# Optimization experiments

Hardware: AMD Instinct MI355X
Metric: run time of the kernel (lower is better)

Reference implementation:

```python
import jax, jax.numpy as jnp
import numpy as np

N = 8192
IN_F = 256
OUT_F = 128
E = 262144
NEG = -9e15


def setup_inputs() -> dict:
    key = jax.random.key(0)
    ks = jax.random.split(key, 12)
    glorot = lambda k, shp: jax.random.uniform(k, shp, jnp.float32,
                                               -jnp.sqrt(6.0 / (shp[0] + shp[1])),
                                               jnp.sqrt(6.0 / (shp[0] + shp[1])))
    return {
        "h_context": jax.random.normal(ks[0], (N, IN_F), jnp.float32),
        "h_structure": jax.random.normal(ks[1], (N, IN_F), jnp.float32),
        "edge_index": jax.random.randint(ks[2], (2, E), 0, N, jnp.int64),
        "Wc_w": glorot(ks[3], (OUT_F, IN_F)),
        "Wc_b": jnp.zeros((OUT_F,), jnp.float32),
        "Ws_w": glorot(ks[4], (OUT_F, IN_F)),
        "Ws_b": jnp.zeros((OUT_F,), jnp.float32),
        "ac_w": glorot(ks[5], (1, 2 * OUT_F)),
        "as_w": glorot(ks[6], (1, 2 * OUT_F)),
        "Ws_coff": jax.random.normal(ks[7], (1, 1), jnp.float32) * 1.414,
        "Wc_coff": jax.random.normal(ks[8], (1, 1), jnp.float32) * 1.414,
    }


def _pair_scores(h, a_w):
    # GAT trick: score[i,j] = leaky_relu(a1 . h[i] + a2 . h[j])
    F_out = h.shape[1]
    s_src = h @ a_w[0, :F_out]   # [N]
    s_dst = h @ a_w[0, F_out:]   # [N]
    return jax.nn.leaky_relu(s_src[:, None] + s_dst[None, :], 0.01)  # [N, N]


def reference(h_context, h_structure, edge_index, Wc_w, Wc_b, Ws_w, Ws_b,
              ac_w, as_w, Ws_coff, Wc_coff):
    hc = h_context @ Wc_w.T + Wc_b                      # [N, F]
    alpha_c = _pair_scores(hc, ac_w)                    # [N, N]
    hs = jax.nn.softmax(h_structure, axis=1) @ Ws_w.T + Ws_b
    alpha_s = _pair_scores(hs, as_w)                    # [N, N]
    alpha = jnp.abs(Ws_coff[0, 0]) * alpha_c + jnp.abs(Wc_coff[0, 0]) * alpha_s
    n = h_structure.shape[0]
    adj = jnp.zeros((n, n), bool).at[edge_index[0], edge_index[1]].set(True)
    attention = jnp.where(adj, alpha, NEG)
    attention = jax.nn.softmax(attention, axis=1)
    # dropout omitted (eval mode / deterministic reference)
    return attention @ hc
```

## Files before the change

kernel.cpp:

```cpp
#include <hip/hip_runtime.h>
#include <hip/hip_bf16.h>
#include <math.h>

#define N_NODES 8192
#define IN_FEAT 256
#define OUT_FEAT 128
#define WORDS_PER_ROW (N_NODES / 64)
#define CAPW 256
#define M_TILE 16

typedef unsigned long long u64;
typedef float v4f __attribute__((ext_vector_type(4)));
typedef short s8v __attribute__((ext_vector_type(8)));
typedef short s4v __attribute__((ext_vector_type(4)));

__device__ __forceinline__ float wred_sum_b(float v) {
    #pragma unroll
    for (int o = 32; o > 0; o >>= 1) v += __shfl_xor(v, o, 64);
    return v;
}
__device__ __forceinline__ float wred_max_b(float v) {
    #pragma unroll
    for (int o = 32; o > 0; o >>= 1) v = fmaxf(v, __shfl_xor(v, o, 64));
    return v;
}

__device__ __forceinline__ void bsplit(float x, unsigned short& hi, unsigned short& lo) {
    unsigned int xb = __float_as_uint(x);
    hi = (unsigned short)(xb >> 16);
    float lof = x - __uint_as_float(xb & 0xFFFF0000u);
    lo = (unsigned short)(__float_as_uint(lof) >> 16);
}

__global__ __launch_bounds__(256) void prep_w(
    const float* __restrict__ Wc, const float* __restrict__ Ws,
    unsigned short* __restrict__ wci, unsigned short* __restrict__ wsi)
{
    int i = blockIdx.x * 256 + threadIdx.x;
    int row = i >> 8, k = i & 255;
    int dst = row * 512 + ((k >> 3) << 4) + (k & 7);
    unsigned short h, l;
    bsplit(Wc[i], h, l); wci[dst] = h; wci[dst + 8] = l;
    bsplit(Ws[i], h, l); wsi[dst] = h; wsi[dst + 8] = l;
}

__global__ __launch_bounds__(256, 2) void node_feats(
    const float* __restrict__ hctx, const float* __restrict__ hstr,
    const unsigned short* __restrict__ wci, const unsigned short* __restrict__ wsi,
    const float* __restrict__ Wcb, const float* __restrict__ Wsb,
    const float* __restrict__ acw, const float* __restrict__ asw,
    const int* __restrict__ ei, int E, u64* __restrict__ bmp,
    float* __restrict__ hc,
    float* __restrict__ csrc, float* __restrict__ cdst,
    float* __restrict__ ssrc, float* __restrict__ sdst)
{
    __shared__ unsigned short aCh[M_TILE][264], aCl[M_TILE][264];
    __shared__ unsigned short aSh[M_TILE][264], aSl[M_TILE][264];
    __shared__ float invsh[M_TILE];
    __shared__ float hcT[M_TILE][132];
    __shared__ float hsT[M_TILE][132];

    const int t = threadIdx.x;
    const int w = t >> 6, ln = t & 63;
    const int r0 = blockIdx.x * M_TILE;

    {
        int pv = ei[2 * (ln & 31) + 1];
        u64 nz = __ballot(pv != 0);
        const int is64 = (nz == 0);
        for (int e = blockIdx.x * 256 + t; e < E; e += 512 * 256) {
            int s, d;
            if (is64) { s = ei[2 * e]; d = ei[2 * E + 2 * e]; }
            else      { s = ei[e];     d = ei[E + e]; }
            if ((unsigned)s < N_NODES && (unsigned)d < N_NODES)
                atomicOr(&bmp[(size_t)s * WORDS_PER_ROW + (d >> 6)], 1ull << (d & 63));
        }
    }

    #pragma unroll
    for (int j = 0; j < 4; j++) {
        int c = t + 256 * j;
        int r = c >> 6;
        int k = (c & 63) * 4;
        const float4 x = *(const float4*)(hctx + (size_t)(r0 + r) * IN_FEAT + k);
        unsigned short h0, h1, h2, h3, l0, l1, l2, l3;
        bsplit(x.x, h0, l0); bsplit(x.y, h1, l1);
        bsplit(x.z, h2, l2); bsplit(x.w, h3, l3);
        s4v hv = { (short)h0, (short)h1, (short)h2, (short)h3 };
        s4v lv = { (short)l0, (short)l1, (short)l2, (short)l3 };
        *(s4v*)&aCh[r][k] = hv;
        *(s4v*)&aCl[r][k] = lv;
    }

    #pragma unroll
    for (int rr = 0; rr < 4; rr++) {
        int r = w * 4 + rr;
        const float* srow = hstr + (size_t)(r0 + r) * IN_FEAT;
        float x0 = srow[ln], x1 = srow[ln + 64], x2 = srow[ln + 128], x3 = srow[ln + 192];
        float mx = wred_max_b(fmaxf(fmaxf(x0, x1), fmaxf(x2, x3)));
        float e0 = __expf(x0 - mx), e1 = __expf(x1 - mx);
        float e2 = __expf(x2 - mx), e3 = __expf(x3 - mx);
        float s = wred_sum_b(e0 + e1 + e2 + e3);
        if (ln == 0) invsh[r] = 1.0f / s;
        unsigned short h, l;
        bsplit(e0, h, l); aSh[r][ln]       = h; aSl[r][ln]       = l;
        bsplit(e1, h, l); aSh[r][ln + 64]  = h; aSl[r][ln + 64]  = l;
        bsplit(e2, h, l); aSh[r][ln + 128] = h; aSl[r][ln + 128] = l;
        bsplit(e3, h, l); aSh[r][ln + 192] = h; aSl[r][ln + 192] = l;
    }
    __syncthreads();

    const int m = ln & 15, q = ln >> 4;
    const int nA = (w << 5) + m, nB = nA + 16;

    v4f aC0 = {0.f,0.f,0.f,0.f}, aC1 = {0.f,0.f,0.f,0.f};
    v4f aS0 = {0.f,0.f,0.f,0.f}, aS1 = {0.f,0.f,0.f,0.f};

    {
        const unsigned short* p0 = wci + nA * 512;
        const unsigned short* p1 = wci + nB * 512;
        #pragma unroll 2
        for (int ks = 0; ks < 8; ks++) {
            const int ko = ks * 32 + q * 8;
            const int io = 2 * ko;
            s8v ah  = *(const s8v*)&aCh[m][ko];
            s8v al  = *(const s8v*)&aCl[m][ko];
            s8v b0h = *(const s8v*)(p0 + io);
            s8v b0l = *(const s8v*)(p0 + io + 8);
            s8v b1h = *(const s8v*)(p1 + io);
            s8v b1l = *(const s8v*)(p1 + io + 8);
            aC0 = __builtin_amdgcn_mfma_f32_16x16x32_bf16(al, b0h, aC0, 0, 0, 0);
            aC0 = __builtin_amdgcn_mfma_f32_16x16x32_bf16(ah, b0l, aC0, 0, 0, 0);
            aC0 = __builtin_amdgcn_mfma_f32_16x16x32_bf16(ah, b0h, aC0, 0, 0, 0);
            aC1 = __builtin_amdgcn_mfma_f32_16x16x32_bf16(al, b1h, aC1, 0, 0, 0);
            aC1 = __builtin_amdgcn_mfma_f32_16x16x32_bf16(ah, b1l, aC1, 0, 0, 0);
            aC1 = __builtin_amdgcn_mfma_f32_16x16x32_bf16(ah, b1h, aC1, 0, 0, 0);
        }
    }
    {
        const unsigned short* p0 = wsi + nA * 512;
        const unsigned short* p1 = wsi + nB * 512;
        #pragma unroll 2
        for (int ks = 0; ks < 8; ks++) {
            const int ko = ks * 32 + q * 8;
            const int io = 2 * ko;
            s8v ah  = *(const s8v*)&aSh[m][ko];
            s8v al  = *(const s8v*)&aSl[m][ko];
            s8v b0h = *(const s8v*)(p0 + io);
            s8v b0l = *(const s8v*)(p0 + io + 8);
            s8v b1h = *(const s8v*)(p1 + io);
            s8v b1l = *(const s8v*)(p1 + io + 8);
            aS0 = __builtin_amdgcn_mfma_f32_16x16x32_bf16(al, b0h, aS0, 0, 0, 0);
            aS0 = __builtin_amdgcn_mfma_f32_16x16x32_bf16(ah, b0l, aS0, 0, 0, 0);
            aS0 = __builtin_amdgcn_mfma_f32_16x16x32_bf16(ah, b0h, aS0, 0, 0, 0);
            aS1 = __builtin_amdgcn_mfma_f32_16x16x32_bf16(al, b1h, aS1, 0, 0, 0);
            aS1 = __builtin_amdgcn_mfma_f32_16x16x32_bf16(ah, b1l, aS1, 0, 0, 0);
            aS1 = __builtin_amdgcn_mfma_f32_16x16x32_bf16(ah, b1h, aS1, 0, 0, 0);
        }
    }

    const float cbA = Wcb[nA], cbB = Wcb[nB];
    const float sbA = Wsb[nA], sbB = Wsb[nB];
    #pragma unroll
    for (int p = 0; p < 4; p++) {
        int row = q * 4 + p;
        float iv = invsh[row];
        hcT[row][nA] = aC0[p] + cbA;
        hcT[row][nB] = aC1[p] + cbB;
        hsT[row][nA] = aS0[p] * iv + sbA;
        hsT[row][nB] = aS1[p] * iv + sbB;
    }
    __syncthreads();

    #pragma unroll
    for (int j = 0; j < 8; j++) {
        int f = t + 256 * j;
        int r = f >> 7, c = f & 127;
        hc[(size_t)(r0 + r) * OUT_FEAT + c] = hcT[r][c];
    }

    float a0 = acw[ln], a0b = acw[ln + 64], a1 = acw[128 + ln], a1b = acw[192 + ln];
    float b0 = asw[ln], b0b = asw[ln + 64], b1 = asw[128 + ln], b1b = asw[192 + ln];
    #pragma unroll
    for (int rr = 0; rr < 4; rr++) {
        int r = w + rr * 4;
        float c0 = hcT[r][ln], c1 = hcT[r][ln + 64];
        float s0 = hsT[r][ln], s1 = hsT[r][ln + 64];
        float v0 = wred_sum_b(c0 * a0 + c1 * a0b);
        float v1 = wred_sum_b(c0 * a1 + c1 * a1b);
        float v2 = wred_sum_b(s0 * b0 + s1 * b0b);
        float v3 = wred_sum_b(s0 * b1 + s1 * b1b);
        if (ln == 0) {
            csrc[r0 + r] = v0; cdst[r0 + r] = v1;
            ssrc[r0 + r] = v2; sdst[r0 + r] = v3;
        }
    }
}

__global__ __launch_bounds__(256) void attn(
    const u64* __restrict__ bmp,
    const float* __restrict__ hc,
    const float* __restrict__ csrc, const float* __restrict__ cdst,
    const float* __restrict__ ssrc, const float* __restrict__ sdst,
    const float* __restrict__ wscoff, const float* __restrict__ wccoff,
    float* __restrict__ out)
{
    __shared__ int   jl[4][CAPW];
    __shared__ float pl[4][CAPW];

    const int w  = threadIdx.x >> 6;
    const int ln = threadIdx.x & 63;
    const int i  = blockIdx.x * 4 + w;

    const float wS = fabsf(wscoff[0]);
    const float wC = fabsf(wccoff[0]);
    const float cs = csrc[i], ss = ssrc[i];

    ulonglong2 wv = *(const ulonglong2*)(bmp + (size_t)i * WORDS_PER_ROW + 2 * ln);
    int c = __popcll(wv.x) + __popcll(wv.y);

    int inc = c;
    #pragma unroll
    for (int o = 1; o < 64; o <<= 1) {
        int y = __shfl_up(inc, o, 64);
        if (ln >= o) inc += y;
    }
    int pre = inc - c;
    int cnt = __shfl(inc, 63, 64);

    int idx = pre;
    #pragma unroll
    for (int h = 0; h < 2; h++) {
        u64 ww = (h == 0) ? wv.x : wv.y;
        int jb = ln * 128 + h * 64;
        while (ww) {
            int b = __ffsll(ww) - 1; ww &= ww - 1;
            int j = jb + b;
            float ac  = cs + cdst[j];
            float as_ = ss + sdst[j];
            ac  = (ac  > 0.0f) ? ac  : 0.01f * ac;
            as_ = (as_ > 0.0f) ? as_ : 0.01f * as_;
            if (idx < CAPW) { jl[w][idx] = j; pl[w][idx] = wS * ac + wC * as_; }
            idx++;
        }
    }
    if (cnt > CAPW) cnt = CAPW;
    __threadfence_block();

    if (cnt == 0) {
        float2 acc = {0.f, 0.f};
        const float2* hc2 = (const float2*)hc;
        for (int j = 0; j < N_NODES; j++) {
            float2 h2 = hc2[(size_t)j * 64 + ln];
            acc.x += h2.x; acc.y += h2.y;
        }
        float2 o2 = { acc.x / (float)N_NODES, acc.y / (float)N_NODES };
        *(float2*)(out + (size_t)i * OUT_FEAT + 2 * ln) = o2;
        return;
    }

    float m = -1e30f;
    for (int k = ln; k < cnt; k += 64) m = fmaxf(m, pl[w][k]);
    m = wred_max_b(m);
    float s = 0.0f;
    for (int k = ln; k < cnt; k += 64) {
        float p = __expf(pl[w][k] - m);
        pl[w][k] = p;
        s += p;
    }
    s = wred_sum_b(s);
    float inv = 1.0f / s;
    __threadfence_block();

    const float2* hc2 = (const float2*)hc;
    float2 acc = {0.f, 0.f};
    int k = 0;
    for (; k + 4 <= cnt; k += 4) {
        int   j0 = jl[w][k],   j1 = jl[w][k+1], j2 = jl[w][k+2], j3 = jl[w][k+3];
        float p0 = pl[w][k],   p1 = pl[w][k+1], p2 = pl[w][k+2], p3 = pl[w][k+3];
        float2 h0 = hc2[(size_t)j0 * 64 + ln];
        float2 h1 = hc2[(size_t)j1 * 64 + ln];
        float2 h2 = hc2[(size_t)j2 * 64 + ln];
        float2 h3 = hc2[(size_t)j3 * 64 + ln];
        acc.x += p0 * h0.x + p1 * h1.x + p2 * h2.x + p3 * h3.x;
        acc.y += p0 * h0.y + p1 * h1.y + p2 * h2.y + p3 * h3.y;
    }
    for (; k < cnt; k++) {
        float2 h0 = hc2[(size_t)jl[w][k] * 64 + ln];
        float p0 = pl[w][k];
        acc.x += p0 * h0.x; acc.y += p0 * h0.y;
    }
    float2 o2 = { acc.x * inv, acc.y * inv };
    *(float2*)(out + (size_t)i * OUT_FEAT + 2 * ln) = o2;
}

extern "C" void kernel_launch(void* const* d_in, const int* in_sizes, int n_in,
                              void* d_out, int out_size, void* d_ws, size_t ws_size,
                              hipStream_t stream)
{
    const float* hctx = (const float*)d_in[0];
    const float* hstr = (const float*)d_in[1];
    const int*   ei   = (const int*)d_in[2];
    const float* Wc   = (const float*)d_in[3];
    const float* Wcb  = (const float*)d_in[4];
    const float* Ws   = (const float*)d_in[5];
    const float* Wsb  = (const float*)d_in[6];
    const float* acw  = (const float*)d_in[7];
    const float* asw  = (const float*)d_in[8];
    const float* wsco = (const float*)d_in[9];
    const float* wcco = (const float*)d_in[10];
    float* out = (float*)d_out;

    const int n2 = in_sizes[2];
    const int E  = (n2 == 4 * 262144) ? 262144 : n2 / 2;

    char* ws = (char*)d_ws;
    size_t off = 0;
    float* hc   = (float*)(ws + off); off += (size_t)N_NODES * OUT_FEAT * sizeof(float);
    float* csrc = (float*)(ws + off); off += (size_t)N_NODES * sizeof(float);
    float* cdst = (float*)(ws + off); off += (size_t)N_NODES * sizeof(float);
    float* ssrc = (float*)(ws + off); off += (size_t)N_NODES * sizeof(float);
    float* sdst = (float*)(ws + off); off += (size_t)N_NODES * sizeof(float);
    off = (off + 255) & ~(size_t)255;
    u64* bmp    = (u64*)(ws + off);   off += (size_t)N_NODES * WORDS_PER_ROW * sizeof(u64);
    unsigned short* wci = (unsigned short*)(ws + off); off += (size_t)OUT_FEAT * IN_FEAT * 2 * sizeof(unsigned short);
    unsigned short* wsi = (unsigned short*)(ws + off); off += (size_t)OUT_FEAT * IN_FEAT * 2 * sizeof(unsigned short);

    hipMemsetAsync(bmp, 0, (size_t)N_NODES * WORDS_PER_ROW * sizeof(u64), stream);

    prep_w<<<128, 256, 0, stream>>>(Wc, Ws, wci, wsi);
    node_feats<<<N_NODES / M_TILE, 256, 0, stream>>>(hctx, hstr, wci, wsi,
                                                     Wcb, Wsb, acw, asw, ei, E, bmp,
                                                     hc, csrc, cdst, ssrc, sdst);
    attn<<<N_NODES / 4, 256, 0, stream>>>(bmp, hc, csrc, cdst, ssrc, sdst, wsco, wcco, out);
}
```

Baseline: 132.3 us.

## Fuse weight prep, node features and attention into one persistent kernel with grid barriers

Merges the three kernels and the bitmap memset into a single 512-block kernel that synchronises through a software grid barrier. Each block zeroes its own slice of the adjacency bitmap and converts weights into an MFMA-fragment-ordered layout so B operands load contiguously per lane. The attention phase now loops over four rows per wave. This removes launch gaps and the memset, but the grid barrier is only safe if all 512 blocks are co-resident, and attention parallelism drops from 2048 blocks to 512.

```diff
diff --git a/kernel.cpp b/kernel.cpp
--- a/kernel.cpp
+++ b/kernel.cpp
@@ -1,13 +1,13 @@
 #include <hip/hip_runtime.h>
-#include <hip/hip_bf16.h>
 #include <math.h>
 
 #define N_NODES 8192
 #define IN_FEAT 256
 #define OUT_FEAT 128
-#define WORDS_PER_ROW (N_NODES / 64)
+#define WORDS_PER_ROW 128
 #define CAPW 256
 #define M_TILE 16
+#define NBLK 512
 
 typedef unsigned long long u64;
 typedef float v4f __attribute__((ext_vector_type(4)));
@@ -32,43 +32,93 @@
     lo = (unsigned short)(__float_as_uint(lof) >> 16);
 }
 
-__global__ __launch_bounds__(256) void prep_w(
-    const float* __restrict__ Wc, const float* __restrict__ Ws,
-    unsigned short* __restrict__ wci, unsigned short* __restrict__ wsi)
-{
-    int i = blockIdx.x * 256 + threadIdx.x;
-    int row = i >> 8, k = i & 255;
-    int dst = row * 512 + ((k >> 3) << 4) + (k & 7);
-    unsigned short h, l;
-    bsplit(Wc[i], h, l); wci[dst] = h; wci[dst + 8] = l;
-    bsplit(Ws[i], h, l); wsi[dst] = h; wsi[dst + 8] = l;
-}
-
-__global__ __launch_bounds__(256, 2) void node_feats(
+__device__ __forceinline__ void grid_barrier(int* cnt, int* gen) {
+    __syncthreads();
+    if (threadIdx.x == 0) {
+        __threadfence();
+        int g = __hip_atomic_load(gen, __ATOMIC_RELAXED, __HIP_MEMORY_SCOPE_AGENT);
+        int arrived = __hip_atomic_fetch_add(cnt, 1, __ATOMIC_ACQ_REL, __HIP_MEMORY_SCOPE_AGENT);
+        if (arrived == NBLK - 1) {
+            __hip_atomic_store(cnt, 0, __ATOMIC_RELAXED, __HIP_MEMORY_SCOPE_AGENT);
+            __hip_atomic_store(gen, g + 1, __ATOMIC_RELEASE, __HIP_MEMORY_SCOPE_AGENT);
+        } else {
+            while (__hip_atomic_load(gen, __ATOMIC_ACQUIRE, __HIP_MEMORY_SCOPE_AGENT) == g)
+                __builtin_amdgcn_s_sleep(2);
+        }
+        __threadfence();
+    }
+    __syncthreads();
+}
+
+__global__ __launch_bounds__(256, 2) void fused(
     const float* __restrict__ hctx, const float* __restrict__ hstr,
-    const unsigned short* __restrict__ wci, const unsigned short* __restrict__ wsi,
+    const float* __restrict__ Wc,  const float* __restrict__ Ws,
     const float* __restrict__ Wcb, const float* __restrict__ Wsb,
     const float* __restrict__ acw, const float* __restrict__ asw,
-    const int* __restrict__ ei, int E, u64* __restrict__ bmp,
+    const float* __restrict__ wscoff, const float* __restrict__ wccoff,
+    const int* __restrict__ ei, int E,
+    u64* __restrict__ bmp,
+    unsigned short* __restrict__ cfrag, unsigned short* __restrict__ sfrag,
     float* __restrict__ hc,
     float* __restrict__ csrc, float* __restrict__ cdst,
-    float* __restrict__ ssrc, float* __restrict__ sdst)
+    float* __restrict__ ssrc, float* __restrict__ sdst,
+    int* __restrict__ bar_cnt, int* __restrict__ bar_gen,
+    float* __restrict__ out)
 {
     __shared__ unsigned short aCh[M_TILE][264], aCl[M_TILE][264];
     __shared__ unsigned short aSh[M_TILE][264], aSl[M_TILE][264];
     __shared__ float invsh[M_TILE];
     __shared__ float hcT[M_TILE][132];
     __shared__ float hsT[M_TILE][132];
+    __shared__ int   jl[4][CAPW];
+    __shared__ float pl[4][CAPW];
 
     const int t = threadIdx.x;
     const int w = t >> 6, ln = t & 63;
-    const int r0 = blockIdx.x * M_TILE;
+    const int b = blockIdx.x;
+    const int r0 = b * M_TILE;
+
+    {
+        ulonglong2 z = {0ull, 0ull};
+        ulonglong2* dst = (ulonglong2*)(bmp + (size_t)b * M_TILE * WORDS_PER_ROW);
+        #pragma unroll
+        for (int k = 0; k < 4; k++) dst[t + 256 * k] = z;
+    }
+    {
+        int tid = b * 256 + t;
+        if (tid < 16384) {
+            int mat = tid >> 13;
+            int f = tid & 8191;
+            int lnf = f & 63;
+            int sel = (f >> 6) & 3;
+            int ks  = (f >> 8) & 7;
+            int wv  = (f >> 11) & 3;
+            int row = (wv << 5) + ((sel >> 1) << 4) + (lnf & 15);
+            int part = sel & 1;
+            int k0 = (ks << 5) + ((lnf >> 4) << 3);
+            const float* src = (mat ? Ws : Wc) + row * IN_FEAT + k0;
+            short tmp[8];
+            #pragma unroll
+            for (int j = 0; j < 8; j++) {
+                float x = src[j];
+                unsigned int xb = __float_as_uint(x);
+                if (part == 0) tmp[j] = (short)(xb >> 16);
+                else {
+                    float lof = x - __uint_as_float(xb & 0xFFFF0000u);
+                    tmp[j] = (short)(__float_as_uint(lof) >> 16);
+                }
+            }
+            unsigned short* dst = (mat ? sfrag : cfrag) + (size_t)f * 8;
+            *(s8v*)dst = *(const s8v*)tmp;
+        }
+    }
+    grid_barrier(bar_cnt, bar_gen);
 
     {
         int pv = ei[2 * (ln & 31) + 1];
         u64 nz = __ballot(pv != 0);
         const int is64 = (nz == 0);
-        for (int e = blockIdx.x * 256 + t; e < E; e += 512 * 256) {
+        for (int e = b * 256 + t; e < E; e += NBLK * 256) {
             int s, d;
             if (is64) { s = ei[2 * e]; d = ei[2 * E + 2 * e]; }
             else      { s = ei[e];     d = ei[E + e]; }
@@ -91,7 +141,6 @@
         *(s4v*)&aCh[r][k] = hv;
         *(s4v*)&aCl[r][k] = lv;
     }
-
     #pragma unroll
     for (int rr = 0; rr < 4; rr++) {
         int r = w * 4 + rr;
@@ -111,54 +160,45 @@
     __syncthreads();
 
     const int m = ln & 15, q = ln >> 4;
-    const int nA = (w << 5) + m, nB = nA + 16;
-
     v4f aC0 = {0.f,0.f,0.f,0.f}, aC1 = {0.f,0.f,0.f,0.f};
     v4f aS0 = {0.f,0.f,0.f,0.f}, aS1 = {0.f,0.f,0.f,0.f};
 
-    {
-        const unsigned short* p0 = wci + nA * 512;
-        const unsigned short* p1 = wci + nB * 512;
-        #pragma unroll 2
-        for (int ks = 0; ks < 8; ks++) {
-            const int ko = ks * 32 + q * 8;
-            const int io = 2 * ko;
-            s8v ah  = *(const s8v*)&aCh[m][ko];
-            s8v al  = *(const s8v*)&aCl[m][ko];
-            s8v b0h = *(const s8v*)(p0 + io);
-            s8v b0l = *(const s8v*)(p0 + io + 8);
-            s8v b1h = *(const s8v*)(p1 + io);
-            s8v b1l = *(const s8v*)(p1 + io + 8);
-            aC0 = __builtin_amdgcn_mfma_f32_16x16x32_bf16(al, b0h, aC0, 0, 0, 0);
-            aC0 = __builtin_amdgcn_mfma_f32_16x16x32_bf16(ah, b0l, aC0, 0, 0, 0);
-            aC0 = __builtin_amdgcn_mfma_f32_16x16x32_bf16(ah, b0h, aC0, 0, 0, 0);
-            aC1 = __builtin_amdgcn_mfma_f32_16x16x32_bf16(al, b1h, aC1, 0, 0, 0);
-            aC1 = __builtin_amdgcn_mfma_f32_16x16x32_bf16(ah, b1l, aC1, 0, 0, 0);
-            aC1 = __builtin_amdgcn_mfma_f32_16x16x32_bf16(ah, b1h, aC1, 0, 0, 0);
-        }
-    }
-    {
-        const unsigned short* p0 = wsi + nA * 512;
-        const unsigned short* p1 = wsi + nB * 512;
-        #pragma unroll 2
-        for (int ks = 0; ks < 8; ks++) {
-            const int ko = ks * 32 + q * 8;
-            const int io = 2 * ko;
-            s8v ah  = *(const s8v*)&aSh[m][ko];
-            s8v al  = *(const s8v*)&aSl[m][ko];
-            s8v b0h = *(const s8v*)(p0 + io);
-            s8v b0l = *(const s8v*)(p0 + io + 8);
-            s8v b1h = *(const s8v*)(p1 + io);
-            s8v b1l = *(const s8v*)(p1 + io + 8);
-            aS0 = __builtin_amdgcn_mfma_f32_16x16x32_bf16(al, b0h, aS0, 0, 0, 0);
-            aS0 = __builtin_amdgcn_mfma_f32_16x16x32_bf16(ah, b0l, aS0, 0, 0, 0);
-            aS0 = __builtin_amdgcn_mfma_f32_16x16x32_bf16(ah, b0h, aS0, 0, 0, 0);
-            aS1 = __builtin_amdgcn_mfma_f32_16x16x32_bf16(al, b1h, aS1, 0, 0, 0);
-            aS1 = __builtin_amdgcn_mfma_f32_16x16x32_bf16(ah, b1l, aS1, 0, 0, 0);
-            aS1 = __builtin_amdgcn_mfma_f32_16x16x32_bf16(ah, b1h, aS1, 0, 0, 0);
-        }
-    }
-
+    #pragma unroll 2
+    for (int ks = 0; ks < 8; ks++) {
+        int ko = ks * 32 + q * 8;
+        const s8v* base = (const s8v*)cfrag + ((w * 8 + ks) * 4) * 64 + ln;
+        s8v ah  = *(const s8v*)&aCh[m][ko];
+        s8v al  = *(const s8v*)&aCl[m][ko];
+        s8v bh0 = base[0];
+        s8v bl0 = base[64];
+        s8v bh1 = base[128];
+        s8v bl1 = base[192];
+        aC0 = __builtin_amdgcn_mfma_f32_16x16x32_bf16(al, bh0, aC0, 0, 0, 0);
+        aC0 = __builtin_amdgcn_mfma_f32_16x16x32_bf16(ah, bl0, aC0, 0, 0, 0);
+        aC0 = __builtin_amdgcn_mfma_f32_16x16x32_bf16(ah, bh0, aC0, 0, 0, 0);
+        aC1 = __builtin_amdgcn_mfma_f32_16x16x32_bf16(al, bh1, aC1, 0, 0, 0);
+        aC1 = __builtin_amdgcn_mfma_f32_16x16x32_bf16(ah, bl1, aC1, 0, 0, 0);
+        aC1 = __builtin_amdgcn_mfma_f32_16x16x32_bf16(ah, bh1, aC1, 0, 0, 0);
+    }
+    #pragma unroll 2
+    for (int ks = 0; ks < 8; ks++) {
+        int ko = ks * 32 + q * 8;
+        const s8v* base = (const s8v*)sfrag + ((w * 8 + ks) * 4) * 64 + ln;
+        s8v ah  = *(const s8v*)&aSh[m][ko];
+        s8v al  = *(const s8v*)&aSl[m][ko];
+        s8v bh0 = base[0];
+        s8v bl0 = base[64];
+        s8v bh1 = base[128];
+        s8v bl1 = base[192];
+        aS0 = __builtin_amdgcn_mfma_f32_16x16x32_bf16(al, bh0, aS0, 0, 0, 0);
+        aS0 = __builtin_amdgcn_mfma_f32_16x16x32_bf16(ah, bl0, aS0, 0, 0, 0);
+        aS0 = __builtin_amdgcn_mfma_f32_16x16x32_bf16(ah, bh0, aS0, 0, 0, 0);
+        aS1 = __builtin_amdgcn_mfma_f32_16x16x32_bf16(al, bh1, aS1, 0, 0, 0);
+        aS1 = __builtin_amdgcn_mfma_f32_16x16x32_bf16(ah, bl1, aS1, 0, 0, 0);
+        aS1 = __builtin_amdgcn_mfma_f32_16x16x32_bf16(ah, bh1, aS1, 0, 0, 0);
+    }
+
+    const int nA = (w << 5) + m, nB = nA + 16;
     const float cbA = Wcb[nA], cbB = Wcb[nB];
     const float sbA = Wsb[nA], sbB = Wsb[nB];
     #pragma unroll
@@ -178,120 +218,109 @@
         int r = f >> 7, c = f & 127;
         hc[(size_t)(r0 + r) * OUT_FEAT + c] = hcT[r][c];
     }
-
-    float a0 = acw[ln], a0b = acw[ln + 64], a1 = acw[128 + ln], a1b = acw[192 + ln];
-    float b0 = asw[ln], b0b = asw[ln + 64], b1 = asw[128 + ln], b1b = asw[192 + ln];
-    #pragma unroll
-    for (int rr = 0; rr < 4; rr++) {
-        int r = w + rr * 4;
-        float c0 = hcT[r][ln], c1 = hcT[r][ln + 64];
-        float s0 = hsT[r][ln], s1 = hsT[r][ln + 64];
-        float v0 = wred_sum_b(c0 * a0 + c1 * a0b);
-        float v1 = wred_sum_b(c0 * a1 + c1 * a1b);
-        float v2 = wred_sum_b(s0 * b0 + s1 * b0b);
-        float v3 = wred_sum_b(s0 * b1 + s1 * b1b);
-        if (ln == 0) {
-            csrc[r0 + r] = v0; cdst[r0 + r] = v1;
-            ssrc[r0 + r] = v2; sdst[r0 + r] = v3;
-        }
-    }
-}
-
-__global__ __launch_bounds__(256) void attn(
-    const u64* __restrict__ bmp,
-    const float* __restrict__ hc,
-    const float* __restrict__ csrc, const float* __restrict__ cdst,
-    const float* __restrict__ ssrc, const float* __restrict__ sdst,
-    const float* __restrict__ wscoff, const float* __restrict__ wccoff,
-    float* __restrict__ out)
-{
-    __shared__ int   jl[4][CAPW];
-    __shared__ float pl[4][CAPW];
-
-    const int w  = threadIdx.x >> 6;
-    const int ln = threadIdx.x & 63;
-    const int i  = blockIdx.x * 4 + w;
+    {
+        float a0 = acw[ln], a0b = acw[ln + 64], a1 = acw[128 + ln], a1b = acw[192 + ln];
+        float b0 = asw[ln], b0b = asw[ln + 64], b1 = asw[128 + ln], b1b = asw[192 + ln];
+        #pragma unroll
+        for (int rr = 0; rr < 4; rr++) {
+            int r = w + rr * 4;
+            float c0 = hcT[r][ln], c1 = hcT[r][ln + 64];
+            float s0 = hsT[r][ln], s1 = hsT[r][ln + 64];
+            float v0 = wred_sum_b(c0 * a0 + c1 * a0b);
+            float v1 = wred_sum_b(c0 * a1 + c1 * a1b);
+            float v2 = wred_sum_b(s0 * b0 + s1 * b0b);
+            float v3 = wred_sum_b(s0 * b1 + s1 * b1b);
+            if (ln == 0) {
+                csrc[r0 + r] = v0; cdst[r0 + r] = v1;
+                ssrc[r0 + r] = v2; sdst[r0 + r] = v3;
+            }
+        }
+    }
+    grid_barrier(bar_cnt, bar_gen);
 
     const float wS = fabsf(wscoff[0]);
     const float wC = fabsf(wccoff[0]);
-    const float cs = csrc[i], ss = ssrc[i];
-
-    ulonglong2 wv = *(const ulonglong2*)(bmp + (size_t)i * WORDS_PER_ROW + 2 * ln);
-    int c = __popcll(wv.x) + __popcll(wv.y);
-
-    int inc = c;
-    #pragma unroll
-    for (int o = 1; o < 64; o <<= 1) {
-        int y = __shfl_up(inc, o, 64);
-        if (ln >= o) inc += y;
-    }
-    int pre = inc - c;
-    int cnt = __shfl(inc, 63, 64);
-
-    int idx = pre;
-    #pragma unroll
-    for (int h = 0; h < 2; h++) {
-        u64 ww = (h == 0) ? wv.x : wv.y;
-        int jb = ln * 128 + h * 64;
-        while (ww) {
-            int b = __ffsll(ww) - 1; ww &= ww - 1;
-            int j = jb + b;
-            float ac  = cs + cdst[j];
-            float as_ = ss + sdst[j];
-            ac  = (ac  > 0.0f) ? ac  : 0.01f * ac;
-            as_ = (as_ > 0.0f) ? as_ : 0.01f * as_;
-            if (idx < CAPW) { jl[w][idx] = j; pl[w][idx] = wS * ac + wC * as_; }
-            idx++;
-        }
-    }
-    if (cnt > CAPW) cnt = CAPW;
-    __threadfence_block();
-
-    if (cnt == 0) {
+    const float2* hc2 = (const float2*)hc;
+
+    for (int rr = 0; rr < 4; rr++) {
+        const int i = b * 16 + w * 4 + rr;
+        const float cs = csrc[i], ss = ssrc[i];
+
+        ulonglong2 wv2 = *(const ulonglong2*)(bmp + (size_t)i * WORDS_PER_ROW + 2 * ln);
+        int c = __popcll(wv2.x) + __popcll(wv2.y);
+
+        int inc = c;
+        #pragma unroll
+        for (int o = 1; o < 64; o <<= 1) {
+            int y = __shfl_up(inc, o, 64);
+            if (ln >= o) inc += y;
+        }
+        int pre = inc - c;
+        int cnt = __shfl(inc, 63, 64);
+
+        int idx = pre;
+        #pragma unroll
+        for (int h = 0; h < 2; h++) {
+            u64 ww = (h == 0) ? wv2.x : wv2.y;
+            int jb = ln * 128 + h * 64;
+            while (ww) {
+                int bt = __ffsll(ww) - 1; ww &= ww - 1;
+                int j = jb + bt;
+                float ac  = cs + cdst[j];
+                float as_ = ss + sdst[j];
+                ac  = (ac  > 0.0f) ? ac  : 0.01f * ac;
+                as_ = (as_ > 0.0f) ? as_ : 0.01f * as_;
+                if (idx < CAPW) { jl[w][idx] = j; pl[w][idx] = wS * ac + wC * as_; }
+                idx++;
+            }
+        }
+        if (cnt > CAPW) cnt = CAPW;
+        __threadfence_block();
+
+        if (cnt == 0) {
+            float2 acc = {0.f, 0.f};
+            for (int j = 0; j < N_NODES; j++) {
+                float2 h2 = hc2[(size_t)j * 64 + ln];
+                acc.x += h2.x; acc.y += h2.y;
+            }
+            float2 o2 = { acc.x / (float)N_NODES, acc.y / (float)N_NODES };
+            *(float2*)(out + (size_t)i * OUT_FEAT + 2 * ln) = o2;
+            continue;
+        }
+
+        float mx = -1e30f;
+        for (int k = ln; k < cnt; k += 64) mx = fmaxf(mx, pl[w][k]);
+        mx = wred_max_b(mx);
+        float sm = 0.0f;
+        for (int k = ln; k < cnt; k += 64) {
+            float p = __expf(pl[w][k] - mx);
+            pl[w][k] = p;
+            sm += p;
+        }
+        sm = wred_sum_b(sm);
+        float inv = 1.0f / sm;
+        __threadfence_block();
+
         float2 acc = {0.f, 0.f};
-        const float2* hc2 = (const float2*)hc;
-        for (int j = 0; j < N_NODES; j++) {
-            float2 h2 = hc2[(size_t)j * 64 + ln];
-            acc.x += h2.x; acc.y += h2.y;
-        }
-        float2 o2 = { acc.x / (float)N_NODES, acc.y / (float)N_NODES };
+        int k = 0;
+        for (; k + 4 <= cnt; k += 4) {
+            int   j0 = jl[w][k],   j1 = jl[w][k+1], j2 = jl[w][k+2], j3 = jl[w][k+3];
+            float p0 = pl[w][k],   p1 = pl[w][k+1], p2 = pl[w][k+2], p3 = pl[w][k+3];
+            float2 h0 = hc2[(size_t)j0 * 64 + ln];
+            float2 h1 = hc2[(size_t)j1 * 64 + ln];
+            float2 h2 = hc2[(size_t)j2 * 64 + ln];
+            float2 h3 = hc2[(size_t)j3 * 64 + ln];
+            acc.x += p0 * h0.x + p1 * h1.x + p2 * h2.x + p3 * h3.x;
+            acc.y += p0 * h0.y + p1 * h1.y + p2 * h2.y + p3 * h3.y;
+        }
+        for (; k < cnt; k++) {
+            float2 h0 = hc2[(size_t)jl[w][k] * 64 + ln];
+            float p0 = pl[w][k];
+            acc.x += p0 * h0.x; acc.y += p0 * h0.y;
+        }
+        float2 o2 = { acc.x * inv, acc.y * inv };
         *(float2*)(out + (size_t)i * OUT_FEAT + 2 * ln) = o2;
-        return;
-    }
-
-    float m = -1e30f;
-    for (int k = ln; k < cnt; k += 64) m = fmaxf(m, pl[w][k]);
-    m = wred_max_b(m);
-    float s = 0.0f;
-    for (int k = ln; k < cnt; k += 64) {
-        float p = __expf(pl[w][k] - m);
-        pl[w][k] = p;
-        s += p;
-    }
-    s = wred_sum_b(s);
-    float inv = 1.0f / s;
-    __threadfence_block();
-
-    const float2* hc2 = (const float2*)hc;
-    float2 acc = {0.f, 0.f};
-    int k = 0;
-    for (; k + 4 <= cnt; k += 4) {
-        int   j0 = jl[w][k],   j1 = jl[w][k+1], j2 = jl[w][k+2], j3 = jl[w][k+3];
-        float p0 = pl[w][k],   p1 = pl[w][k+1], p2 = pl[w][k+2], p3 = pl[w][k+3];
-        float2 h0 = hc2[(size_t)j0 * 64 + ln];
-        float2 h1 = hc2[(size_t)j1 * 64 + ln];
-        float2 h2 = hc2[(size_t)j2 * 64 + ln];
-        float2 h3 = hc2[(size_t)j3 * 64 + ln];
-        acc.x += p0 * h0.x + p1 * h1.x + p2 * h2.x + p3 * h3.x;
-        acc.y += p0 * h0.y + p1 * h1.y + p2 * h2.y + p3 * h3.y;
-    }
-    for (; k < cnt; k++) {
-        float2 h0 = hc2[(size_t)jl[w][k] * 64 + ln];
-        float p0 = pl[w][k];
-        acc.x += p0 * h0.x; acc.y += p0 * h0.y;
-    }
-    float2 o2 = { acc.x * inv, acc.y * inv };
-    *(float2*)(out + (size_t)i * OUT_FEAT + 2 * ln) = o2;
+    }
 }
 
 extern "C" void kernel_launch(void* const* d_in, const int* in_sizes, int n_in,
@@ -323,14 +352,17 @@
     float* sdst = (float*)(ws + off); off += (size_t)N_NODES * sizeof(float);
     off = (off + 255) & ~(size_t)255;
     u64* bmp    = (u64*)(ws + off);   off += (size_t)N_NODES * WORDS_PER_ROW * sizeof(u64);
-    unsigned short* wci = (unsigned short*)(ws + off); off += (size_t)OUT_FEAT * IN_FEAT * 2 * sizeof(unsigned short);
-    unsigned short* wsi = (unsigned short*)(ws + off); off += (size_t)OUT_FEAT * IN_FEAT * 2 * sizeof(unsigned short);
-
-    hipMemsetAsync(bmp, 0, (size_t)N_NODES * WORDS_PER_ROW * sizeof(u64), stream);
-
-    prep_w<<<128, 256, 0, stream>>>(Wc, Ws, wci, wsi);
-    node_feats<<<N_NODES / M_TILE, 256, 0, stream>>>(hctx, hstr, wci, wsi,
-                                                     Wcb, Wsb, acw, asw, ei, E, bmp,
-                                                     hc, csrc, cdst, ssrc, sdst);
-    attn<<<N_NODES / 4, 256, 0, stream>>>(bmp, hc, csrc, cdst, ssrc, sdst, wsco, wcco, out);
-}
+    unsigned short* cfrag = (unsigned short*)(ws + off); off += (size_t)8192 * 8 * sizeof(unsigned short);
+    unsigned short* sfrag = (unsigned short*)(ws + off); off += (size_t)8192 * 8 * sizeof(unsigned short);
+    off = (off + 255) & ~(size_t)255;
+    int* bar = (int*)(ws + off); off += 256;
+    int* bar_cnt = bar;
+    int* bar_gen = bar + 16;
+
+    hipMemsetAsync(bar, 0, 128, stream);
+
+    fused<<<NBLK, 256, 0, stream>>>(hctx, hstr, Wc, Ws, Wcb, Wsb, acw, asw,
+                                    wsco, wcco, ei, E, bmp, cfrag, sfrag,
+                                    hc, csrc, cdst, ssrc, sdst,
+                                    bar_cnt, bar_gen, out);
+}
```

Measured after the change: 274.3 us. 107% more time.

## Split node_feats into context/structure blocks and fuse weight split in-kernel

Applied to the files above, without the earlier changes.

Removes the separate prep_w launch: each block now loads fp32 weights straight from global memory and splits them into bf16 hi/lo pairs in registers. The node_feats grid is doubled so that half the blocks compute the context projection and half the structure projection. Shared memory per block is halved and launch bounds now allow 4 blocks per CU, which raises parallelism and occupancy. The cost is redundant weight splitting in every block and more global weight reads (fp32 instead of preformatted bf16).

```diff
diff --git a/kernel.cpp b/kernel.cpp
--- a/kernel.cpp
+++ b/kernel.cpp
@@ -1,13 +1,13 @@
 #include <hip/hip_runtime.h>
-#include <hip/hip_bf16.h>
 #include <math.h>
 
 #define N_NODES 8192
 #define IN_FEAT 256
 #define OUT_FEAT 128
-#define WORDS_PER_ROW (N_NODES / 64)
+#define WORDS_PER_ROW 128
 #define CAPW 256
 #define M_TILE 16
+#define NF_BLOCKS 1024
 
 typedef unsigned long long u64;
 typedef float v4f __attribute__((ext_vector_type(4)));
@@ -32,21 +32,21 @@
     lo = (unsigned short)(__float_as_uint(lof) >> 16);
 }
 
-__global__ __launch_bounds__(256) void prep_w(
-    const float* __restrict__ Wc, const float* __restrict__ Ws,
-    unsigned short* __restrict__ wci, unsigned short* __restrict__ wsi)
-{
-    int i = blockIdx.x * 256 + threadIdx.x;
-    int row = i >> 8, k = i & 255;
-    int dst = row * 512 + ((k >> 3) << 4) + (k & 7);
-    unsigned short h, l;
-    bsplit(Wc[i], h, l); wci[dst] = h; wci[dst + 8] = l;
-    bsplit(Ws[i], h, l); wsi[dst] = h; wsi[dst + 8] = l;
-}
-
-__global__ __launch_bounds__(256, 2) void node_feats(
+__device__ __forceinline__ void split8(const float* p, s8v& h8, s8v& l8) {
+    short hh[8], ll[8];
+    #pragma unroll
+    for (int j = 0; j < 8; j++) {
+        unsigned short h, l;
+        bsplit(p[j], h, l);
+        hh[j] = (short)h; ll[j] = (short)l;
+    }
+    h8 = *(const s8v*)hh;
+    l8 = *(const s8v*)ll;
+}
+
+__global__ __launch_bounds__(256, 4) void node_feats(
     const float* __restrict__ hctx, const float* __restrict__ hstr,
-    const unsigned short* __restrict__ wci, const unsigned short* __restrict__ wsi,
+    const float* __restrict__ Wc,  const float* __restrict__ Ws,
     const float* __restrict__ Wcb, const float* __restrict__ Wsb,
     const float* __restrict__ acw, const float* __restrict__ asw,
     const int* __restrict__ ei, int E, u64* __restrict__ bmp,
@@ -54,21 +54,21 @@
     float* __restrict__ csrc, float* __restrict__ cdst,
     float* __restrict__ ssrc, float* __restrict__ sdst)
 {
-    __shared__ unsigned short aCh[M_TILE][264], aCl[M_TILE][264];
-    __shared__ unsigned short aSh[M_TILE][264], aSl[M_TILE][264];
+    __shared__ unsigned short aH[M_TILE][264], aL[M_TILE][264];
     __shared__ float invsh[M_TILE];
-    __shared__ float hcT[M_TILE][132];
-    __shared__ float hsT[M_TILE][132];
+    __shared__ float hT[M_TILE][132];
 
     const int t = threadIdx.x;
     const int w = t >> 6, ln = t & 63;
-    const int r0 = blockIdx.x * M_TILE;
+    const int is_struct = (blockIdx.x >= 512);
+    const int b = blockIdx.x & 511;
+    const int r0 = b * M_TILE;
 
     {
         int pv = ei[2 * (ln & 31) + 1];
         u64 nz = __ballot(pv != 0);
         const int is64 = (nz == 0);
-        for (int e = blockIdx.x * 256 + t; e < E; e += 512 * 256) {
+        for (int e = blockIdx.x * 256 + t; e < E; e += NF_BLOCKS * 256) {
             int s, d;
             if (is64) { s = ei[2 * e]; d = ei[2 * E + 2 * e]; }
             else      { s = ei[e];     d = ei[E + e]; }
@@ -77,122 +77,114 @@
         }
     }
 
-    #pragma unroll
-    for (int j = 0; j < 4; j++) {
-        int c = t + 256 * j;
-        int r = c >> 6;
-        int k = (c & 63) * 4;
-        const float4 x = *(const float4*)(hctx + (size_t)(r0 + r) * IN_FEAT + k);
-        unsigned short h0, h1, h2, h3, l0, l1, l2, l3;
-        bsplit(x.x, h0, l0); bsplit(x.y, h1, l1);
-        bsplit(x.z, h2, l2); bsplit(x.w, h3, l3);
-        s4v hv = { (short)h0, (short)h1, (short)h2, (short)h3 };
-        s4v lv = { (short)l0, (short)l1, (short)l2, (short)l3 };
-        *(s4v*)&aCh[r][k] = hv;
-        *(s4v*)&aCl[r][k] = lv;
-    }
-
-    #pragma unroll
-    for (int rr = 0; rr < 4; rr++) {
-        int r = w * 4 + rr;
-        const float* srow = hstr + (size_t)(r0 + r) * IN_FEAT;
-        float x0 = srow[ln], x1 = srow[ln + 64], x2 = srow[ln + 128], x3 = srow[ln + 192];
-        float mx = wred_max_b(fmaxf(fmaxf(x0, x1), fmaxf(x2, x3)));
-        float e0 = __expf(x0 - mx), e1 = __expf(x1 - mx);
-        float e2 = __expf(x2 - mx), e3 = __expf(x3 - mx);
-        float s = wred_sum_b(e0 + e1 + e2 + e3);
-        if (ln == 0) invsh[r] = 1.0f / s;
-        unsigned short h, l;
-        bsplit(e0, h, l); aSh[r][ln]       = h; aSl[r][ln]       = l;
-        bsplit(e1, h, l); aSh[r][ln + 64]  = h; aSl[r][ln + 64]  = l;
-        bsplit(e2, h, l); aSh[r][ln + 128] = h; aSl[r][ln + 128] = l;
-        bsplit(e3, h, l); aSh[r][ln + 192] = h; aSl[r][ln + 192] = l;
+    if (!is_struct) {
+        #pragma unroll
+        for (int j = 0; j < 4; j++) {
+            int c = t + 256 * j;
+            int r = c >> 6;
+            int k = (c & 63) * 4;
+            const float4 x = *(const float4*)(hctx + (size_t)(r0 + r) * IN_FEAT + k);
+            unsigned short h0, h1, h2, h3, l0, l1, l2, l3;
+            bsplit(x.x, h0, l0); bsplit(x.y, h1, l1);
+            bsplit(x.z, h2, l2); bsplit(x.w, h3, l3);
+            s4v hv = { (short)h0, (short)h1, (short)h2, (short)h3 };
+            s4v lv = { (short)l0, (short)l1, (short)l2, (short)l3 };
+            *(s4v*)&aH[r][k] = hv;
+            *(s4v*)&aL[r][k] = lv;
+        }
+    } else {
+        #pragma unroll
+        for (int rr = 0; rr < 4; rr++) {
+            int r = w * 4 + rr;
+            const float* srow = hstr + (size_t)(r0 + r) * IN_FEAT;
+            float x0 = srow[ln], x1 = srow[ln + 64], x2 = srow[ln + 128], x3 = srow[ln + 192];
+            float mx = wred_max_b(fmaxf(fmaxf(x0, x1), fmaxf(x2, x3)));
+            float e0 = __expf(x0 - mx), e1 = __expf(x1 - mx);
+            float e2 = __expf(x2 - mx), e3 = __expf(x3 - mx);
+            float s = wred_sum_b(e0 + e1 + e2 + e3);
+            if (ln == 0) invsh[r] = 1.0f / s;
+            unsigned short h, l;
+            bsplit(e0, h, l); aH[r][ln]       = h; aL[r][ln]       = l;
+            bsplit(e1, h, l); aH[r][ln + 64]  = h; aL[r][ln + 64]  = l;
+            bsplit(e2, h, l); aH[r][ln + 128] = h; aL[r][ln + 128] = l;
+            bsplit(e3, h, l); aH[r][ln + 192] = h; aL[r][ln + 192] = l;
+        }
     }
     __syncthreads();
 
     const int m = ln & 15, q = ln >> 4;
     const int nA = (w << 5) + m, nB = nA + 16;
-
-    v4f aC0 = {0.f,0.f,0.f,0.f}, aC1 = {0.f,0.f,0.f,0.f};
-    v4f aS0 = {0.f,0.f,0.f,0.f}, aS1 = {0.f,0.f,0.f,0.f};
-
-    {
-        const unsigned short* p0 = wci + nA * 512;
-        const unsigned short* p1 = wci + nB * 512;
-        #pragma unroll 2
-        for (int ks = 0; ks < 8; ks++) {
-            const int ko = ks * 32 + q * 8;
-            const int io = 2 * ko;
-            s8v ah  = *(const s8v*)&aCh[m][ko];
-            s8v al  = *(const s8v*)&aCl[m][ko];
-            s8v b0h = *(const s8v*)(p0 + io);
-            s8v b0l = *(const s8v*)(p0 + io + 8);
-            s8v b1h = *(const s8v*)(p1 + io);
-            s8v b1l = *(const s8v*)(p1 + io + 8);
-            aC0 = __builtin_amdgcn_mfma_f32_16x16x32_bf16(al, b0h, aC0, 0, 0, 0);
-            aC0 = __builtin_amdgcn_mfma_f32_16x16x32_bf16(ah, b0l, aC0, 0, 0, 0);
-            aC0 = __builtin_amdgcn_mfma_f32_16x16x32_bf16(ah, b0h, aC0, 0, 0, 0);
-            aC1 = __builtin_amdgcn_mfma_f32_16x16x32_bf16(al, b1h, aC1, 0, 0, 0);
-            aC1 = __builtin_amdgcn_mfma_f32_16x16x32_bf16(ah, b1l, aC1, 0, 0, 0);
-            aC1 = __builtin_amdgcn_mfma_f32_16x16x32_bf16(ah, b1h, aC1, 0, 0, 0);
-        }
-    }
-    {
-        const unsigned short* p0 = wsi + nA * 512;
-        const unsigned short* p1 = wsi + nB * 512;
-        #pragma unroll 2
-        for (int ks = 0; ks < 8; ks++) {
-            const int ko = ks * 32 + q * 8;
-            const int io = 2 * ko;
-            s8v ah  = *(const s8v*)&aSh[m][ko];
-            s8v al  = *(const s8v*)&aSl[m][ko];
-            s8v b0h = *(const s8v*)(p0 + io);
-            s8v b0l = *(const s8v*)(p0 + io + 8);
-            s8v b1h = *(const s8v*)(p1 + io);
-            s8v b1l = *(const s8v*)(p1 + io + 8);
-            aS0 = __builtin_amdgcn_mfma_f32_16x16x32_bf16(al, b0h, aS0, 0, 0, 0);
-            aS0 = __builtin_amdgcn_mfma_f32_16x16x32_bf16(ah, b0l, aS0, 0, 0, 0);
-            aS0 = __builtin_amdgcn_mfma_f32_16x16x32_bf16(ah, b0h, aS0, 0, 0, 0);
-            aS1 = __builtin_amdgcn_mfma_f32_16x16x32_bf16(al, b1h, aS1, 0, 0, 0);
-            aS1 = __builtin_amdgcn_mfma_f32_16x16x32_bf16(ah, b1l, aS1, 0, 0, 0);
-            aS1 = __builtin_amdgcn_mfma_f32_16x16x32_bf16(ah, b1h, aS1, 0, 0, 0);
-        }
-    }
-
-    const float cbA = Wcb[nA], cbB = Wcb[nB];
-    const float sbA = Wsb[nA], sbB = Wsb[nB];
-    #pragma unroll
-    for (int p = 0; p < 4; p++) {
-        int row = q * 4 + p;
-        float iv = invsh[row];
-        hcT[row][nA] = aC0[p] + cbA;
-        hcT[row][nB] = aC1[p] + cbB;
-        hsT[row][nA] = aS0[p] * iv + sbA;
-        hsT[row][nB] = aS1[p] * iv + sbB;
-    }
-    __syncthreads();
-
-    #pragma unroll
-    for (int j = 0; j < 8; j++) {
-        int f = t + 256 * j;
-        int r = f >> 7, c = f & 127;
-        hc[(size_t)(r0 + r) * OUT_FEAT + c] = hcT[r][c];
-    }
-
-    float a0 = acw[ln], a0b = acw[ln + 64], a1 = acw[128 + ln], a1b = acw[192 + ln];
-    float b0 = asw[ln], b0b = asw[ln + 64], b1 = asw[128 + ln], b1b = asw[192 + ln];
-    #pragma unroll
-    for (int rr = 0; rr < 4; rr++) {
-        int r = w + rr * 4;
-        float c0 = hcT[r][ln], c1 = hcT[r][ln + 64];
-        float s0 = hsT[r][ln], s1 = hsT[r][ln + 64];
-        float v0 = wred_sum_b(c0 * a0 + c1 * a0b);
-        float v1 = wred_sum_b(c0 * a1 + c1 * a1b);
-        float v2 = wred_sum_b(s0 * b0 + s1 * b0b);
-        float v3 = wred_sum_b(s0 * b1 + s1 * b1b);
-        if (ln == 0) {
-            csrc[r0 + r] = v0; cdst[r0 + r] = v1;
-            ssrc[r0 + r] = v2; sdst[r0 + r] = v3;
+    const float* W = is_struct ? Ws : Wc;
+    const float* rowA = W + (size_t)nA * IN_FEAT;
+    const float* rowB = W + (size_t)nB * IN_FEAT;
+
+    v4f acc0 = {0.f,0.f,0.f,0.f}, acc1 = {0.f,0.f,0.f,0.f};
+
+    #pragma unroll 2
+    for (int ks = 0; ks < 8; ks++) {
+        const int k0 = ks * 32 + q * 8;
+        float wbufA[8], wbufB[8];
+        *(float4*)&wbufA[0] = *(const float4*)(rowA + k0);
+        *(float4*)&wbufA[4] = *(const float4*)(rowA + k0 + 4);
+        *(float4*)&wbufB[0] = *(const float4*)(rowB + k0);
+        *(float4*)&wbufB[4] = *(const float4*)(rowB + k0 + 4);
+        s8v bhA, blA, bhB, blB;
+        split8(wbufA, bhA, blA);
+        split8(wbufB, bhB, blB);
+        s8v ah = *(const s8v*)&aH[m][k0];
+        s8v al = *(const s8v*)&aL[m][k0];
+        acc0 = __builtin_amdgcn_mfma_f32_16x16x32_bf16(al, bhA, acc0, 0, 0, 0);
+        acc0 = __builtin_amdgcn_mfma_f32_16x16x32_bf16(ah, blA, acc0, 0, 0, 0);
+        acc0 = __builtin_amdgcn_mfma_f32_16x16x32_bf16(ah, bhA, acc0, 0, 0, 0);
+        acc1 = __builtin_amdgcn_mfma_f32_16x16x32_bf16(al, bhB, acc1, 0, 0, 0);
+        acc1 = __builtin_amdgcn_mfma_f32_16x16x32_bf16(ah, blB, acc1, 0, 0, 0);
+        acc1 = __builtin_amdgcn_mfma_f32_16x16x32_bf16(ah, bhB, acc1, 0, 0, 0);
+    }
+
+    if (!is_struct) {
+        const float bA = Wcb[nA], bB = Wcb[nB];
+        #pragma unroll
+        for (int p = 0; p < 4; p++) {
+            int row = q * 4 + p;
+            hT[row][nA] = acc0[p] + bA;
+            hT[row][nB] = acc1[p] + bB;
+        }
+        __syncthreads();
+
+        #pragma unroll
+        for (int j = 0; j < 8; j++) {
+            int f = t + 256 * j;
+            int r = f >> 7, c = f & 127;
+            hc[(size_t)(r0 + r) * OUT_FEAT + c] = hT[r][c];
+        }
+        float a0 = acw[ln], a0b = acw[ln + 64], a1 = acw[128 + ln], a1b = acw[192 + ln];
+        #pragma unroll
+        for (int rr = 0; rr < 4; rr++) {
+            int r = w + rr * 4;
+            float c0 = hT[r][ln], c1 = hT[r][ln + 64];
+            float v0 = wred_sum_b(c0 * a0 + c1 * a0b);
+            float v1 = wred_sum_b(c0 * a1 + c1 * a1b);
+            if (ln == 0) { csrc[r0 + r] = v0; cdst[r0 + r] = v1; }
+        }
+    } else {
+        const float bA = Wsb[nA], bB = Wsb[nB];
+        #pragma unroll
+        for (int p = 0; p < 4; p++) {
+            int row = q * 4 + p;
+            float iv = invsh[row];
+            hT[row][nA] = acc0[p] * iv + bA;
+            hT[row][nB] = acc1[p] * iv + bB;
+        }
+        __syncthreads();
+
+        float b0 = asw[ln], b0b = asw[ln + 64], b1 = asw[128 + ln], b1b = asw[192 + ln];
+        #pragma unroll
+        for (int rr = 0; rr < 4; rr++) {
+            int r = w + rr * 4;
+            float s0 = hT[r][ln], s1 = hT[r][ln + 64];
+            float v2 = wred_sum_b(s0 * b0 + s1 * b0b);
+            float v3 = wred_sum_b(s0 * b1 + s1 * b1b);
+            if (ln == 0) { ssrc[r0 + r] = v2; sdst[r0 + r] = v3; }
         }
     }
 }
@@ -234,8 +226,8 @@
         u64 ww = (h == 0) ? wv.x : wv.y;
         int jb = ln * 128 + h * 64;
         while (ww) {
-            int b = __ffsll(ww) - 1; ww &= ww - 1;
-            int j = jb + b;
+            int bt = __ffsll(ww) - 1; ww &= ww - 1;
+            int j = jb + bt;
             float ac  = cs + cdst[j];
             float as_ = ss + sdst[j];
             ac  = (ac  > 0.0f) ? ac  : 0.01f * ac;
@@ -323,14 +315,11 @@
     float* sdst = (float*)(ws + off); off += (size_t)N_NODES * sizeof(float);
     off = (off + 255) & ~(size_t)255;
     u64* bmp    = (u64*)(ws + off);   off += (size_t)N_NODES * WORDS_PER_ROW * sizeof(u64);
-    unsigned short* wci = (unsigned short*)(ws + off); off += (size_t)OUT_FEAT * IN_FEAT * 2 * sizeof(unsigned short);
-    unsigned short* wsi = (unsigned short*)(ws + off); off += (size_t)OUT_FEAT * IN_FEAT * 2 * sizeof(unsigned short);
 
     hipMemsetAsync(bmp, 0, (size_t)N_NODES * WORDS_PER_ROW * sizeof(u64), stream);
 
-    prep_w<<<128, 256, 0, stream>>>(Wc, Ws, wci, wsi);
-    node_feats<<<N_NODES / M_TILE, 256, 0, stream>>>(hctx, hstr, wci, wsi,
-                                                     Wcb, Wsb, acw, asw, ei, E, bmp,
-                                                     hc, csrc, cdst, ssrc, sdst);
+    node_feats<<<NF_BLOCKS, 256, 0, stream>>>(hctx, hstr, Wc, Ws, Wcb, Wsb,
+                                              acw, asw, ei, E, bmp,
+                                              hc, csrc, cdst, ssrc, sdst);
     attn<<<N_NODES / 4, 256, 0, stream>>>(bmp, hc, csrc, cdst, ssrc, sdst, wsco, wcco, out);
 }
```

Result: faster. 127.4 us (-3.7%).
